# Optimization experiments

Measured on AMD Instinct MI355X. Metric: run time of the kernel, lower is better.

The kernel has to match this reference:

```python
import jax, jax.numpy as jnp
import numpy as np

N_LINEARS = 16
CHANNELS = 3
OUTPUT_DIM = 64
Z_DIM = 128
BATCH = 512


def hash_vectors(z, n):
    # Deterministic surrogate for repo's hash_vectors: map each latent vector
    # to an integer bucket in [0, n). Data-dependent, jit-compatible.
    s = jnp.abs(jnp.sum(z, axis=1)) * 1000.0
    return jnp.mod(jnp.floor(s).astype(jnp.int32), n)


def setup_inputs() -> dict:
    key = jax.random.key(0)
    k1, k2, k3 = jax.random.split(key, 3)
    out_features = CHANNELS * OUTPUT_DIM ** 2 * N_LINEARS  # 196608
    z = jax.random.normal(k1, (BATCH, Z_DIM), dtype=jnp.float32)
    # Linear weight stored as (out_features, in_features), torch convention.
    W = jax.random.normal(k2, (out_features, Z_DIM), dtype=jnp.float32) * (1.0 / np.sqrt(Z_DIM))
    b = jax.random.normal(k3, (out_features,), dtype=jnp.float32) * 0.01
    return {"z": z, "W": W, "b": b}


def reference(z, W, b):
    B = z.shape[0]
    # Dense GEMM: (B, out_features)
    out = jnp.einsum('bi,oi->bo', z, W) + b
    out = out.reshape(B, N_LINEARS, CHANNELS, OUTPUT_DIM, OUTPUT_DIM)
    c = hash_vectors(z, N_LINEARS)  # (B,) int32 in [0, N_LINEARS)
    # Per-sample gather of one linear's output block.
    return jnp.take_along_axis(out, c[:, None, None, None, None], axis=1)[:, 0]
```

## Files before the change

### kernel.cpp

```cpp
#include <hip/hip_runtime.h>
#include <hip/hip_bf16.h>
#include <math.h>


#define N_LINEARS 16
#define ZD 128
#define BATCH 512
#define BLOCK_OUT 12288
#define STILE 48
#define SLOTS 64
#define ZROWS (ZD + 1)
#define TJ 256

typedef float vf16 __attribute__((ext_vector_type(16)));
typedef vf16 vf16u __attribute__((aligned(16)));

#define LISTS_OFF 16
#define BP_OFF (36864 / 4)
#define ZG_OFF_BYTES 65536

__global__ __launch_bounds__(512) void hash_kernel(
    const float* __restrict__ z, int* __restrict__ counts,
    int* __restrict__ lists, int* __restrict__ bp) {
  __shared__ int cnt[N_LINEARS];
  const int b = threadIdx.x;
  if (b < N_LINEARS) cnt[b] = 0;
  __syncthreads();

  const float4* zr4 = (const float4*)(z + b * ZD);
  const float4 pa = zr4[0], pb = zr4[1];
  float r0 = pa.x, r1 = pa.y, r2 = pa.z, r3 = pa.w;
  float r4 = pb.x, r5 = pb.y, r6 = pb.z, r7 = pb.w;
  #pragma unroll
  for (int i = 2; i < ZD / 4; i += 2) {
    const float4 a = zr4[i], d = zr4[i + 1];
    r0 += a.x; r1 += a.y; r2 += a.z; r3 += a.w;
    r4 += d.x; r5 += d.y; r6 += d.z; r7 += d.w;
  }
  float res = ((r0 + r1) + (r2 + r3)) + ((r4 + r5) + (r6 + r7));
  float v = fabsf(res) * 1000.0f;
  int cb = ((int)floorf(v)) & (N_LINEARS - 1);

  int pos = atomicAdd(&cnt[cb], 1);
  lists[(cb << 9) + pos] = b;
  bp[b] = cb | (pos << 4);

  __syncthreads();
  if (b < N_LINEARS) counts[b] = cnt[b];
}

__global__ __launch_bounds__(128) void gather_kernel(
    const float* __restrict__ z, const int* __restrict__ bp,
    float* __restrict__ zgT) {
  const int b = blockIdx.x;
  const int k = threadIdx.x;
  const int v = bp[b];
  const int cb = v & 15;
  const int pos = v >> 4;
  if (pos < SLOTS)
    zgT[(size_t)cb * (ZROWS * SLOTS) + (size_t)k * SLOTS + pos] = z[b * ZD + k];
}


#define ZLOAD(N0, N1, N2, K1)                                        \
  { const int zo_ = (K1) * SLOTS + s0;                               \
    N0 = *(const vf16u*)&zsh[zo_];                                   \
    N1 = *(const vf16u*)&zsh[zo_ + 16];                              \
    N2 = *(const vf16u*)&zsh[zo_ + 32]; }

#define ZFMA(C0, C1, C2, WK)                                         \
  { const float wk_ = (WK);                                          \
    vf16 wv_;                                                        \
    _Pragma("unroll") for (int e = 0; e < 16; ++e) wv_[e] = wk_;     \
    acc0 += C0 * wv_; acc1 += C1 * wv_; acc2 += C2 * wv_; }

#define STEP(C0, C1, C2, N0, N1, N2, K1, WK)                         \
  ZLOAD(N0, N1, N2, K1) ZFMA(C0, C1, C2, WK)

__global__ __launch_bounds__(TJ, 3) void gen_main_kernel(
    const float* __restrict__ W, const float* __restrict__ bias,
    float* __restrict__ out, const int* __restrict__ counts,
    const int* __restrict__ lists, const float* __restrict__ zgT) {
  __shared__ float zsh[ZD * SLOTS + 32 + 64];
  const int c = blockIdx.y;
  const int j = blockIdx.x * TJ + threadIdx.x;
  int n = counts[c];
  n = n > SLOTS ? SLOTS : n;
  if (n == 0) return;

  {
    const float4* zg4 = (const float4*)(zgT + (size_t)c * (ZROWS * SLOTS));
    float4* ls4 = (float4*)zsh;
    #pragma unroll
    for (int i = 0; i < 8; ++i) {
      const int idx = threadIdx.x + i * TJ;
      ls4[idx] = zg4[idx];
    }
  }
  __syncthreads();

  const size_t row = (size_t)c * BLOCK_OUT + (size_t)j;
  const float4* __restrict__ Wv = (const float4*)(W + row * (size_t)ZD);
  const float bj = bias[row];
  const int* __restrict__ lst = lists + (c << 9);

  for (int s0 = 0; s0 < n; s0 += STILE) {
    const int m = n - s0;
    vf16 acc0, acc1, acc2;
    #pragma unroll
    for (int e = 0; e < 16; ++e) { acc0[e] = bj; acc1[e] = bj; acc2[e] = bj; }

    vf16 zA0, zA1, zA2, zB0, zB1, zB2;
    ZLOAD(zA0, zA1, zA2, 0)
    float4 w0 = Wv[0];
    float4 w1 = Wv[1];
    float4 w2 = Wv[2];
    float4 w3 = Wv[3];

    #pragma unroll 4
    for (int kc = 0; kc < ZD / 4; ++kc) {
      const int k0 = kc * 4;
      STEP(zA0, zA1, zA2, zB0, zB1, zB2, k0 + 1, w0.x)
      STEP(zB0, zB1, zB2, zA0, zA1, zA2, k0 + 2, w0.y)
      STEP(zA0, zA1, zA2, zB0, zB1, zB2, k0 + 3, w0.z)
      STEP(zB0, zB1, zB2, zA0, zA1, zA2, k0 + 4, w0.w)
      w0 = w1; w1 = w2; w2 = w3;
      const int wi = kc + 4 > 31 ? 31 : kc + 4;
      w3 = Wv[wi];
    }

    #pragma unroll
    for (int t = 0; t < 16; ++t)
      if (t < m) out[(size_t)lst[s0 + t] * BLOCK_OUT + j] = acc0[t];
    #pragma unroll
    for (int t = 0; t < 16; ++t)
      if (16 + t < m) out[(size_t)lst[s0 + 16 + t] * BLOCK_OUT + j] = acc1[t];
    #pragma unroll
    for (int t = 0; t < 16; ++t)
      if (32 + t < m) out[(size_t)lst[s0 + 32 + t] * BLOCK_OUT + j] = acc2[t];
  }
}

extern "C" void kernel_launch(void* const* d_in, const int* in_sizes, int n_in,
                              void* d_out, int out_size, void* d_ws, size_t ws_size,
                              hipStream_t stream) {
  const float* z    = (const float*)d_in[0];
  const float* W    = (const float*)d_in[1];
  const float* bias = (const float*)d_in[2];
  float* out = (float*)d_out;

  int*   counts = (int*)d_ws;
  int*   lists  = (int*)d_ws + LISTS_OFF;
  int*   bp     = (int*)d_ws + BP_OFF;
  float* zgT    = (float*)((char*)d_ws + ZG_OFF_BYTES);

  hipLaunchKernelGGL(hash_kernel, dim3(1), dim3(BATCH), 0, stream,
                     z, counts, lists, bp);
  hipLaunchKernelGGL(gather_kernel, dim3(BATCH), dim3(ZD), 0, stream,
                     z, bp, zgT);

  dim3 grid(BLOCK_OUT / TJ, N_LINEARS);
  hipLaunchKernelGGL(gen_main_kernel, grid, dim3(TJ), 0, stream,
                     W, bias, out, counts, lists, zgT);
}
```

Before: 188.8 us.

## Map samples to lanes and broadcast W rows, dropping the gather kernel

Each of the 64 lanes now handles one sample of its bucket and keeps that sample's z row (128 floats) in registers. Every lane reads the same W rows, four output rows per iteration, so the loads are broadcast, and each lane writes a float4 to its own output row. This removes the separate gather kernel and the shared-memory staging of z. The cost is a 128-register z array per thread, a small 64-thread block, W reads not coalesced across lanes, and output stores scattered by sample.

```diff
diff --git a/kernel.cpp b/kernel.cpp
--- a/kernel.cpp
+++ b/kernel.cpp
@@ -7,21 +7,16 @@
 #define ZD 128
 #define BATCH 512
 #define BLOCK_OUT 12288
-#define STILE 48
 #define SLOTS 64
-#define ZROWS (ZD + 1)
-#define TJ 256
+#define NJW 64
 
-typedef float vf16 __attribute__((ext_vector_type(16)));
-typedef vf16 vf16u __attribute__((aligned(16)));
+typedef float vf2 __attribute__((ext_vector_type(2)));
 
 #define LISTS_OFF 16
-#define BP_OFF (36864 / 4)
-#define ZG_OFF_BYTES 65536
 
 __global__ __launch_bounds__(512) void hash_kernel(
     const float* __restrict__ z, int* __restrict__ counts,
-    int* __restrict__ lists, int* __restrict__ bp) {
+    int* __restrict__ lists) {
   __shared__ int cnt[N_LINEARS];
   const int b = threadIdx.x;
   if (b < N_LINEARS) cnt[b] = 0;
@@ -42,102 +37,62 @@
   int cb = ((int)floorf(v)) & (N_LINEARS - 1);
 
   int pos = atomicAdd(&cnt[cb], 1);
-  lists[(cb << 9) + pos] = b;
-  bp[b] = cb | (pos << 4);
+  if (pos < SLOTS) lists[(cb << 9) + pos] = b;
 
   __syncthreads();
   if (b < N_LINEARS) counts[b] = cnt[b];
 }
 
-__global__ __launch_bounds__(128) void gather_kernel(
-    const float* __restrict__ z, const int* __restrict__ bp,
-    float* __restrict__ zgT) {
-  const int b = blockIdx.x;
-  const int k = threadIdx.x;
-  const int v = bp[b];
-  const int cb = v & 15;
-  const int pos = v >> 4;
-  if (pos < SLOTS)
-    zgT[(size_t)cb * (ZROWS * SLOTS) + (size_t)k * SLOTS + pos] = z[b * ZD + k];
-}
 
-
-#define ZLOAD(N0, N1, N2, K1)                                        \
-  { const int zo_ = (K1) * SLOTS + s0;                               \
-    N0 = *(const vf16u*)&zsh[zo_];                                   \
-    N1 = *(const vf16u*)&zsh[zo_ + 16];                              \
-    N2 = *(const vf16u*)&zsh[zo_ + 32]; }
-
-#define ZFMA(C0, C1, C2, WK)                                         \
-  { const float wk_ = (WK);                                          \
-    vf16 wv_;                                                        \
-    _Pragma("unroll") for (int e = 0; e < 16; ++e) wv_[e] = wk_;     \
-    acc0 += C0 * wv_; acc1 += C1 * wv_; acc2 += C2 * wv_; }
-
-#define STEP(C0, C1, C2, N0, N1, N2, K1, WK)                         \
-  ZLOAD(N0, N1, N2, K1) ZFMA(C0, C1, C2, WK)
-
-__global__ __launch_bounds__(TJ, 3) void gen_main_kernel(
+__global__ __launch_bounds__(64, 3) void gen_main_kernel(
     const float* __restrict__ W, const float* __restrict__ bias,
     float* __restrict__ out, const int* __restrict__ counts,
-    const int* __restrict__ lists, const float* __restrict__ zgT) {
-  __shared__ float zsh[ZD * SLOTS + 32 + 64];
+    const int* __restrict__ lists, const float* __restrict__ z) {
   const int c = blockIdx.y;
-  const int j = blockIdx.x * TJ + threadIdx.x;
+  const int l = threadIdx.x;
   int n = counts[c];
   n = n > SLOTS ? SLOTS : n;
   if (n == 0) return;
 
-  {
-    const float4* zg4 = (const float4*)(zgT + (size_t)c * (ZROWS * SLOTS));
-    float4* ls4 = (float4*)zsh;
+  const bool act = l < n;
+  const int sample = act ? lists[(c << 9) + l] : 0;
+  float* __restrict__ outp = out + (size_t)sample * BLOCK_OUT;
+
+  const float4* __restrict__ zp = (const float4*)(z + (size_t)sample * ZD);
+  float4 zr[32];
+  #pragma unroll
+  for (int i = 0; i < 32; ++i) zr[i] = zp[i];
+
+  const int j0 = blockIdx.x * NJW;
+  const size_t rowbase = (size_t)c * BLOCK_OUT + (size_t)j0;
+
+  for (int jj = 0; jj < NJW; jj += 4) {
+    const size_t row = rowbase + jj;
+    const float* __restrict__ Wr = W + row * (size_t)ZD;
+    const float4 b4 = *(const float4*)(bias + row);
+
+    vf2 a0 = {b4.x, 0.0f}, a1 = {b4.y, 0.0f};
+    vf2 a2 = {b4.z, 0.0f}, a3 = {b4.w, 0.0f};
+
     #pragma unroll
-    for (int i = 0; i < 8; ++i) {
-      const int idx = threadIdx.x + i * TJ;
-      ls4[idx] = zg4[idx];
-    }
-  }
-  __syncthreads();
-
-  const size_t row = (size_t)c * BLOCK_OUT + (size_t)j;
-  const float4* __restrict__ Wv = (const float4*)(W + row * (size_t)ZD);
-  const float bj = bias[row];
-  const int* __restrict__ lst = lists + (c << 9);
-
-  for (int s0 = 0; s0 < n; s0 += STILE) {
-    const int m = n - s0;
-    vf16 acc0, acc1, acc2;
-    #pragma unroll
-    for (int e = 0; e < 16; ++e) { acc0[e] = bj; acc1[e] = bj; acc2[e] = bj; }
-
-    vf16 zA0, zA1, zA2, zB0, zB1, zB2;
-    ZLOAD(zA0, zA1, zA2, 0)
-    float4 w0 = Wv[0];
-    float4 w1 = Wv[1];
-    float4 w2 = Wv[2];
-    float4 w3 = Wv[3];
-
-    #pragma unroll 4
-    for (int kc = 0; kc < ZD / 4; ++kc) {
-      const int k0 = kc * 4;
-      STEP(zA0, zA1, zA2, zB0, zB1, zB2, k0 + 1, w0.x)
-      STEP(zB0, zB1, zB2, zA0, zA1, zA2, k0 + 2, w0.y)
-      STEP(zA0, zA1, zA2, zB0, zB1, zB2, k0 + 3, w0.z)
-      STEP(zB0, zB1, zB2, zA0, zA1, zA2, k0 + 4, w0.w)
-      w0 = w1; w1 = w2; w2 = w3;
-      const int wi = kc + 4 > 31 ? 31 : kc + 4;
-      w3 = Wv[wi];
+    for (int kq = 0; kq < 32; ++kq) {
+      const float4 w0 = *(const float4*)(Wr + kq * 4);
+      const float4 w1 = *(const float4*)(Wr + ZD + kq * 4);
+      const float4 w2 = *(const float4*)(Wr + 2 * ZD + kq * 4);
+      const float4 w3 = *(const float4*)(Wr + 3 * ZD + kq * 4);
+      const float4 z4 = zr[kq];
+      const vf2 zlo = {z4.x, z4.y};
+      const vf2 zhi = {z4.z, z4.w};
+      a0 += (vf2){w0.x, w0.y} * zlo;  a0 += (vf2){w0.z, w0.w} * zhi;
+      a1 += (vf2){w1.x, w1.y} * zlo;  a1 += (vf2){w1.z, w1.w} * zhi;
+      a2 += (vf2){w2.x, w2.y} * zlo;  a2 += (vf2){w2.z, w2.w} * zhi;
+      a3 += (vf2){w3.x, w3.y} * zlo;  a3 += (vf2){w3.z, w3.w} * zhi;
     }
 
-    #pragma unroll
-    for (int t = 0; t < 16; ++t)
-      if (t < m) out[(size_t)lst[s0 + t] * BLOCK_OUT + j] = acc0[t];
-    #pragma unroll
-    for (int t = 0; t < 16; ++t)
-      if (16 + t < m) out[(size_t)lst[s0 + 16 + t] * BLOCK_OUT + j] = acc1[t];
-    #pragma unroll
-    for (int t = 0; t < 16; ++t)
-      if (32 + t < m) out[(size_t)lst[s0 + 32 + t] * BLOCK_OUT + j] = acc2[t];
+    if (act) {
+      const float4 o = {a0.x + a0.y, a1.x + a1.y, a2.x + a2.y, a3.x + a3.y};
+      *(float4*)(outp + j0 + jj) = o;
+    }
   }
 }
 
@@ -149,17 +104,13 @@
   const float* bias = (const float*)d_in[2];
   float* out = (float*)d_out;
 
-  int*   counts = (int*)d_ws;
-  int*   lists  = (int*)d_ws + LISTS_OFF;
-  int*   bp     = (int*)d_ws + BP_OFF;
-  float* zgT    = (float*)((char*)d_ws + ZG_OFF_BYTES);
+  int* counts = (int*)d_ws;
+  int* lists  = (int*)d_ws + LISTS_OFF;
 
   hipLaunchKernelGGL(hash_kernel, dim3(1), dim3(BATCH), 0, stream,
-                     z, counts, lists, bp);
-  hipLaunchKernelGGL(gather_kernel, dim3(BATCH), dim3(ZD), 0, stream,
-                     z, bp, zgT);
+                     z, counts, lists);
 
-  dim3 grid(BLOCK_OUT / TJ, N_LINEARS);
-  hipLaunchKernelGGL(gen_main_kernel, grid, dim3(TJ), 0, stream,
-                     W, bias, out, counts, lists, zgT);
+  dim3 grid(BLOCK_OUT / NJW, N_LINEARS);
+  hipLaunchKernelGGL(gen_main_kernel, grid, dim3(64), 0, stream,
+                     W, bias, out, counts, lists, z);
 }
```

After: 386.6 us. +104.7%, slower.
